# Performance work log

Hardware: AMD Instinct MI355X
Metric: run time of the kernel (lower is better)

## Reference

```python
import jax, jax.numpy as jnp
import numpy as np


def setup_inputs() -> dict:
    key = jax.random.key(0)
    kE, kD, kW, kU, kV = jax.random.split(key, 5)
    B, T, H, U = 32, 2048, 1024, 1024
    scale = 0.02
    return {
        "enc_out": jax.random.normal(kE, (B, T, H), dtype=jnp.float32),
        "dec_hidden": jax.random.normal(kD, (B, H), dtype=jnp.float32),
        "Wa": jax.random.normal(kW, (H, U), dtype=jnp.float32) * scale,
        "Ua": jax.random.normal(kU, (H, U), dtype=jnp.float32) * scale,
        "Va": jax.random.normal(kV, (U,), dtype=jnp.float32) * scale,
    }


def reference(enc_out, dec_hidden, Wa, Ua, Va):
    # Bahdanau additive attention.
    # enc_out: [B, T, H]; dec_hidden: [B, H]; Wa: [H, U]; Ua: [H, U]; Va: [U]
    dec_proj = jnp.einsum("bh,hu->bu", dec_hidden, Wa)          # [B, U]
    enc_proj = jnp.einsum("bth,hu->btu", enc_out, Ua)            # [B, T, U]
    s = jnp.tanh(enc_proj + dec_proj[:, None, :])                # [B, T, U]
    score = jnp.einsum("btu,u->bt", s, Va)                       # [B, T]
    alpha = jax.nn.softmax(score, axis=-1)                       # [B, T]
    context = jnp.einsum("bt,bth->bh", alpha, enc_out)           # [B, H]
    return context
```

## Files before the change

kernel.cpp:

```cpp
#include <hip/hip_runtime.h>
#include <stdint.h>


#define B_ 32
#define T_ 2048
#define H_ 1024
#define U_ 1024
#define M_ (B_ * T_)

typedef __bf16 bf16x8 __attribute__((ext_vector_type(8)));
typedef float f32x4 __attribute__((ext_vector_type(4)));

__device__ __forceinline__ unsigned f2b(float f) {
  unsigned u = __float_as_uint(f);
  return (u + 0x7FFFu + ((u >> 16) & 1u)) >> 16;
}
__device__ __forceinline__ float b2f(unsigned short u) {
  return __uint_as_float(((unsigned)u) << 16);
}
__device__ __forceinline__ float fast_tanh(float x) {
  float xc = fminf(fmaxf(x, -12.f), 12.f);
  float t = exp2f(xc * 2.885390081777927f);
  return (t - 1.f) * __builtin_amdgcn_rcpf(t + 1.f);
}

#define AS1 __attribute__((address_space(1)))
#define AS3 __attribute__((address_space(3)))
__device__ __forceinline__ void gld_lds16(const void* g, void* l) {
  __builtin_amdgcn_global_load_lds((AS1 const void*)g, (AS3 void*)l, 16, 0, 0);
}

__global__ __launch_bounds__(256) void conv_enc_k(const float4* __restrict__ in,
                                                  uint4* __restrict__ outA) {
  const int ml = threadIdx.x & 127, kh = threadIdx.x >> 7;
  const int bk = blockIdx.x;
  const int mt = blockIdx.y;
  const int kc = bk * 2 + kh;
  const float4* src = in + ((size_t)(mt * 128 + ml) * 256) + kc * 4;
  float4 a = src[0], b = src[1], c = src[2], d = src[3];
  uint4 o0, o1;
  o0.x = f2b(a.x) | (f2b(a.y) << 16);
  o0.y = f2b(a.z) | (f2b(a.w) << 16);
  o0.z = f2b(b.x) | (f2b(b.y) << 16);
  o0.w = f2b(b.z) | (f2b(b.w) << 16);
  o1.x = f2b(c.x) | (f2b(c.y) << 16);
  o1.y = f2b(c.z) | (f2b(c.w) << 16);
  o1.z = f2b(d.x) | (f2b(d.y) << 16);
  o1.w = f2b(d.z) | (f2b(d.w) << 16);
  const int k8 = kc * 2;
  outA[((size_t)mt * 128 + k8) * 128 + ml] = o0;
  outA[((size_t)mt * 128 + k8 + 1) * 128 + ml] = o1;
}

__global__ __launch_bounds__(256) void conv_ua_k(const float* __restrict__ in,
                                                 unsigned short* __restrict__ out) {
  int id = blockIdx.x * 256 + threadIdx.x;
  int h = id >> 10, u = id & 1023;
  out[(((size_t)(h >> 3) * U_ + u) << 3) + (h & 7)] = (unsigned short)f2b(in[id]);
}

__global__ __launch_bounds__(256) void decproj_k(const float* __restrict__ dh,
                                                 const float* __restrict__ Wa,
                                                 float* __restrict__ dp) {
  const int u = blockIdx.x * 256 + threadIdx.x;
  const int b = blockIdx.y, hz = blockIdx.z;
  const float* d = dh + b * H_ + hz * 256;
  const float* w = Wa + (size_t)(hz * 256) * U_ + u;
  float a0 = 0.f, a1 = 0.f, a2 = 0.f, a3 = 0.f;
#pragma unroll 4
  for (int h = 0; h < 256; h += 4) {
    a0 = fmaf(d[h + 0], w[(size_t)(h + 0) * U_], a0);
    a1 = fmaf(d[h + 1], w[(size_t)(h + 1) * U_], a1);
    a2 = fmaf(d[h + 2], w[(size_t)(h + 2) * U_], a2);
    a3 = fmaf(d[h + 3], w[(size_t)(h + 3) * U_], a3);
  }
  atomicAdd(&dp[b * U_ + u], (a0 + a1) + (a2 + a3));
}

__global__ __launch_bounds__(256, 2) void score_gemm_k(
    const unsigned short* __restrict__ encA,
    const unsigned short* __restrict__ Ub,
    const float* __restrict__ dp,
    const float* __restrict__ Va,
    float* __restrict__ score)
{
  __shared__ union {
    struct {
      alignas(16) unsigned short As[8][128][8];
      alignas(16) unsigned short Bs[8][128][8];
    } t;
    float sred[128 * 33];
  } sm;

  const int bx = blockIdx.x;
  const int mtile = bx & 511, ntile = bx >> 9;
  const int m0 = mtile << 7, n0 = ntile << 7;
  const int tid = threadIdx.x;
  const int wv = tid >> 6, ln = tid & 63;
  const int wm = wv & 1, wn = wv >> 1;
  const int quad = ln >> 4, l16 = ln & 15;

  f32x4 acc[4][4];
  const f32x4 zero = {0.f, 0.f, 0.f, 0.f};
#pragma unroll
  for (int i = 0; i < 4; ++i)
#pragma unroll
    for (int j = 0; j < 4; ++j) acc[i][j] = zero;

  const unsigned short* encT = encA + (size_t)mtile * (128 * 128 * 8);

  for (int k0 = 0; k0 < H_; k0 += 64) {
    __syncthreads();
#pragma unroll
    for (int c = 0; c < 4; ++c) {
      int chunk = (wv << 2) + c;
      int k8 = chunk >> 1, half = chunk & 1;
      const unsigned short* ga =
          encT + (((size_t)((k0 >> 3) + k8) * 128) + (half << 6) + ln) * 8;
      gld_lds16(ga, &sm.t.As[k8][half << 6][0]);
      const unsigned short* gb =
          Ub + (((size_t)((k0 >> 3) + k8) * U_) + n0 + (half << 6) + ln) * 8;
      gld_lds16(gb, &sm.t.Bs[k8][half << 6][0]);
    }
    __syncthreads();

#pragma unroll
    for (int kk = 0; kk < 2; ++kk) {
      int k8b = (kk << 2) + quad;
      bf16x8 af[4], bf[4];
#pragma unroll
      for (int mt = 0; mt < 4; ++mt)
        af[mt] = *(const bf16x8*)&sm.t.As[k8b][(wm << 6) + (mt << 4) + l16][0];
#pragma unroll
      for (int nt = 0; nt < 4; ++nt)
        bf[nt] = *(const bf16x8*)&sm.t.Bs[k8b][(wn << 6) + (nt << 4) + l16][0];
#pragma unroll
      for (int mt = 0; mt < 4; ++mt)
#pragma unroll
        for (int nt = 0; nt < 4; ++nt)
          acc[mt][nt] = __builtin_amdgcn_mfma_f32_16x16x32_bf16(
              af[mt], bf[nt], acc[mt][nt], 0, 0, 0);
    }
  }

  const int bq = m0 >> 11;
  float va[4], dpv[4];
#pragma unroll
  for (int nt = 0; nt < 4; ++nt) {
    int col = n0 + (wn << 6) + (nt << 4) + l16;
    va[nt] = Va[col];
    dpv[nt] = dp[bq * U_ + col];
  }
  __syncthreads();
#pragma unroll
  for (int mt = 0; mt < 4; ++mt) {
#pragma unroll
    for (int r = 0; r < 4; ++r) {
      float v = 0.f;
#pragma unroll
      for (int nt = 0; nt < 4; ++nt)
        v += fast_tanh(acc[mt][nt][r] + dpv[nt]) * va[nt];
      int row = (wm << 6) + (mt << 4) + (quad << 2) + r;
      sm.sred[row * 33 + (wn << 4) + l16] = v;
    }
  }
  __syncthreads();
  if (tid < 128) {
    const float* p = &sm.sred[tid * 33];
    float s = 0.f;
#pragma unroll
    for (int j = 0; j < 32; ++j) s += p[j];
    atomicAdd(&score[m0 + tid], s);
  }
}

__global__ __launch_bounds__(256) void softmax_k(float* __restrict__ score) {
  const int b = blockIdx.x, tid = threadIdx.x;
  float4* s4 = (float4*)(score + b * T_);
  __shared__ float red[4];
  float4 v0 = s4[tid * 2], v1 = s4[tid * 2 + 1];
  float m = fmaxf(fmaxf(fmaxf(v0.x, v0.y), fmaxf(v0.z, v0.w)),
                  fmaxf(fmaxf(v1.x, v1.y), fmaxf(v1.z, v1.w)));
#pragma unroll
  for (int off = 32; off >= 1; off >>= 1) m = fmaxf(m, __shfl_xor(m, off));
  if ((tid & 63) == 0) red[tid >> 6] = m;
  __syncthreads();
  m = fmaxf(fmaxf(red[0], red[1]), fmaxf(red[2], red[3]));
  __syncthreads();
  const float l2e = 1.4426950408889634f;
  float e[8];
  e[0] = exp2f((v0.x - m) * l2e); e[1] = exp2f((v0.y - m) * l2e);
  e[2] = exp2f((v0.z - m) * l2e); e[3] = exp2f((v0.w - m) * l2e);
  e[4] = exp2f((v1.x - m) * l2e); e[5] = exp2f((v1.y - m) * l2e);
  e[6] = exp2f((v1.z - m) * l2e); e[7] = exp2f((v1.w - m) * l2e);
  float sum = (e[0] + e[1]) + (e[2] + e[3]) + (e[4] + e[5]) + (e[6] + e[7]);
#pragma unroll
  for (int off = 32; off >= 1; off >>= 1) sum += __shfl_xor(sum, off);
  if ((tid & 63) == 0) red[tid >> 6] = sum;
  __syncthreads();
  float inv = 1.f / (red[0] + red[1] + red[2] + red[3]);
  v0.x = e[0] * inv; v0.y = e[1] * inv; v0.z = e[2] * inv; v0.w = e[3] * inv;
  v1.x = e[4] * inv; v1.y = e[5] * inv; v1.z = e[6] * inv; v1.w = e[7] * inv;
  s4[tid * 2] = v0;
  s4[tid * 2 + 1] = v1;
}

__global__ __launch_bounds__(256) void context_k(const uint4* __restrict__ encA,
                                                 const float* __restrict__ alpha,
                                                 float* __restrict__ out) {
  const int tx = threadIdx.x & 127, th = threadIdx.x >> 7;
  const int b = blockIdx.y, bt = blockIdx.x;
  const int mt = b * 16 + bt;
  const uint4* base = encA + ((size_t)mt * 128 + tx) * 128 + th * 64;
  const float* al = alpha + b * T_ + bt * 128 + th * 64;
  float a[8];
#pragma unroll
  for (int j = 0; j < 8; ++j) a[j] = 0.f;
#pragma unroll 4
  for (int i = 0; i < 64; ++i) {
    float w = al[i];
    uint4 e = base[i];
    a[0] = fmaf(w, b2f((unsigned short)e.x), a[0]);
    a[1] = fmaf(w, b2f((unsigned short)(e.x >> 16)), a[1]);
    a[2] = fmaf(w, b2f((unsigned short)e.y), a[2]);
    a[3] = fmaf(w, b2f((unsigned short)(e.y >> 16)), a[3]);
    a[4] = fmaf(w, b2f((unsigned short)e.z), a[4]);
    a[5] = fmaf(w, b2f((unsigned short)(e.z >> 16)), a[5]);
    a[6] = fmaf(w, b2f((unsigned short)e.w), a[6]);
    a[7] = fmaf(w, b2f((unsigned short)(e.w >> 16)), a[7]);
  }
  __shared__ float cred[2][128][8];
#pragma unroll
  for (int j = 0; j < 8; ++j) cred[th][tx][j] = a[j];
  __syncthreads();
  if (th == 0) {
#pragma unroll
    for (int j = 0; j < 8; ++j)
      atomicAdd(&out[b * H_ + tx * 8 + j], cred[0][tx][j] + cred[1][tx][j]);
  }
}

extern "C" void kernel_launch(void* const* d_in, const int* in_sizes, int n_in,
                              void* d_out, int out_size, void* d_ws, size_t ws_size,
                              hipStream_t stream) {
  const float* enc = (const float*)d_in[0];
  const float* dh  = (const float*)d_in[1];
  const float* Wa  = (const float*)d_in[2];
  const float* Ua  = (const float*)d_in[3];
  const float* Va  = (const float*)d_in[4];

  char* ws = (char*)d_ws;
  unsigned short* encA = (unsigned short*)ws;
  unsigned short* Ub   = (unsigned short*)(ws + 134217728);
  float* dp    = (float*)(ws + 134217728 + 2097152);
  float* score = (float*)(ws + 134217728 + 2097152 + 131072);

  hipMemsetAsync(dp, 0, B_ * U_ * sizeof(float), stream);
  hipMemsetAsync(score, 0, M_ * sizeof(float), stream);
  hipMemsetAsync(d_out, 0, B_ * H_ * sizeof(float), stream);

  conv_enc_k<<<dim3(32, 512), 256, 0, stream>>>((const float4*)enc, (uint4*)encA);
  conv_ua_k<<<4096, 256, 0, stream>>>(Ua, Ub);
  decproj_k<<<dim3(4, 32, 4), 256, 0, stream>>>(dh, Wa, dp);
  score_gemm_k<<<4096, 256, 0, stream>>>(encA, Ub, dp, Va, score);
  softmax_k<<<32, 256, 0, stream>>>(score);
  context_k<<<dim3(16, 32), 256, 0, stream>>>((const uint4*)encA, score, (float*)d_out);
}
```

Measured before the change: 626.9 us.

## Replace atomics with partial buffers and coalesce encoder bf16 conversion via LDS

Rewrites the encoder fp32-to-bf16 conversion so each block reads contiguous rows and writes the blocked layout through an LDS transpose, giving coalesced stores. All atomicAdd reductions (decoder projection, scores, context) are replaced by writes to per-split partial buffers that later kernels sum. This removes the three memsets and atomic contention, at the cost of an extra reduction kernel and more partial-buffer traffic. The workspace regions are reused: alpha aliases dp4 and ctxp aliases score8.

```diff
diff --git a/kernel.cpp b/kernel.cpp
--- a/kernel.cpp
+++ b/kernel.cpp
@@ -32,24 +32,32 @@
 
 __global__ __launch_bounds__(256) void conv_enc_k(const float4* __restrict__ in,
                                                   uint4* __restrict__ outA) {
-  const int ml = threadIdx.x & 127, kh = threadIdx.x >> 7;
-  const int bk = blockIdx.x;
-  const int mt = blockIdx.y;
-  const int kc = bk * 2 + kh;
-  const float4* src = in + ((size_t)(mt * 128 + ml) * 256) + kc * 4;
-  float4 a = src[0], b = src[1], c = src[2], d = src[3];
-  uint4 o0, o1;
-  o0.x = f2b(a.x) | (f2b(a.y) << 16);
-  o0.y = f2b(a.z) | (f2b(a.w) << 16);
-  o0.z = f2b(b.x) | (f2b(b.y) << 16);
-  o0.w = f2b(b.z) | (f2b(b.w) << 16);
-  o1.x = f2b(c.x) | (f2b(c.y) << 16);
-  o1.y = f2b(c.z) | (f2b(c.w) << 16);
-  o1.z = f2b(d.x) | (f2b(d.y) << 16);
-  o1.w = f2b(d.z) | (f2b(d.w) << 16);
-  const int k8 = kc * 2;
-  outA[((size_t)mt * 128 + k8) * 128 + ml] = o0;
-  outA[((size_t)mt * 128 + k8 + 1) * 128 + ml] = o1;
+  __shared__ uint4 L4[128 * 17];
+  const int tx = threadIdx.x;
+  const int band = blockIdx.x;
+  const int mt = band >> 3;
+  const int R = (band & 7) << 4;
+  const float4* src = in + (size_t)band * 4096;
+#pragma unroll
+  for (int i = 0; i < 8; ++i) {
+    int p = i * 256 + tx;
+    int r = p >> 7, pc = p & 127;
+    float4 a = src[r * 256 + pc * 2];
+    float4 b = src[r * 256 + pc * 2 + 1];
+    uint4 o;
+    o.x = f2b(a.x) | (f2b(a.y) << 16);
+    o.y = f2b(a.z) | (f2b(a.w) << 16);
+    o.z = f2b(b.x) | (f2b(b.y) << 16);
+    o.w = f2b(b.z) | (f2b(b.w) << 16);
+    L4[pc * 17 + r] = o;
+  }
+  __syncthreads();
+  const int r2 = tx & 15, kq = (tx >> 4) & 3, w = tx >> 6;
+#pragma unroll
+  for (int j = 0; j < 8; ++j) {
+    int k8 = j * 16 + w * 4 + kq;
+    outA[((size_t)mt * 128 + k8) * 128 + R + r2] = L4[k8 * 17 + r2];
+  }
 }
 
 __global__ __launch_bounds__(256) void conv_ua_k(const float* __restrict__ in,
@@ -61,7 +69,7 @@
 
 __global__ __launch_bounds__(256) void decproj_k(const float* __restrict__ dh,
                                                  const float* __restrict__ Wa,
-                                                 float* __restrict__ dp) {
+                                                 float* __restrict__ dp4) {
   const int u = blockIdx.x * 256 + threadIdx.x;
   const int b = blockIdx.y, hz = blockIdx.z;
   const float* d = dh + b * H_ + hz * 256;
@@ -74,15 +82,15 @@
     a2 = fmaf(d[h + 2], w[(size_t)(h + 2) * U_], a2);
     a3 = fmaf(d[h + 3], w[(size_t)(h + 3) * U_], a3);
   }
-  atomicAdd(&dp[b * U_ + u], (a0 + a1) + (a2 + a3));
+  dp4[((hz * B_ + b) * U_) + u] = (a0 + a1) + (a2 + a3);
 }
 
 __global__ __launch_bounds__(256, 2) void score_gemm_k(
     const unsigned short* __restrict__ encA,
     const unsigned short* __restrict__ Ub,
-    const float* __restrict__ dp,
+    const float* __restrict__ dp4,
     const float* __restrict__ Va,
-    float* __restrict__ score)
+    float* __restrict__ score8)
 {
   __shared__ union {
     struct {
@@ -149,7 +157,8 @@
   for (int nt = 0; nt < 4; ++nt) {
     int col = n0 + (wn << 6) + (nt << 4) + l16;
     va[nt] = Va[col];
-    dpv[nt] = dp[bq * U_ + col];
+    dpv[nt] = dp4[bq * U_ + col] + dp4[B_ * U_ + bq * U_ + col] +
+              dp4[2 * B_ * U_ + bq * U_ + col] + dp4[3 * B_ * U_ + bq * U_ + col];
   }
   __syncthreads();
 #pragma unroll
@@ -170,15 +179,22 @@
     float s = 0.f;
 #pragma unroll
     for (int j = 0; j < 32; ++j) s += p[j];
-    atomicAdd(&score[m0 + tid], s);
-  }
-}
-
-__global__ __launch_bounds__(256) void softmax_k(float* __restrict__ score) {
+    score8[(size_t)ntile * M_ + m0 + tid] = s;
+  }
+}
+
+__global__ __launch_bounds__(256) void softmax_k(const float* __restrict__ score8,
+                                                 float* __restrict__ alpha) {
   const int b = blockIdx.x, tid = threadIdx.x;
-  float4* s4 = (float4*)(score + b * T_);
   __shared__ float red[4];
-  float4 v0 = s4[tid * 2], v1 = s4[tid * 2 + 1];
+  float4 v0 = {0.f, 0.f, 0.f, 0.f}, v1 = {0.f, 0.f, 0.f, 0.f};
+#pragma unroll
+  for (int k = 0; k < 8; ++k) {
+    const float4* p = (const float4*)(score8 + (size_t)k * M_ + b * T_);
+    float4 x0 = p[tid * 2], x1 = p[tid * 2 + 1];
+    v0.x += x0.x; v0.y += x0.y; v0.z += x0.z; v0.w += x0.w;
+    v1.x += x1.x; v1.y += x1.y; v1.z += x1.z; v1.w += x1.w;
+  }
   float m = fmaxf(fmaxf(fmaxf(v0.x, v0.y), fmaxf(v0.z, v0.w)),
                   fmaxf(fmaxf(v1.x, v1.y), fmaxf(v1.z, v1.w)));
 #pragma unroll
@@ -199,15 +215,17 @@
   if ((tid & 63) == 0) red[tid >> 6] = sum;
   __syncthreads();
   float inv = 1.f / (red[0] + red[1] + red[2] + red[3]);
-  v0.x = e[0] * inv; v0.y = e[1] * inv; v0.z = e[2] * inv; v0.w = e[3] * inv;
-  v1.x = e[4] * inv; v1.y = e[5] * inv; v1.z = e[6] * inv; v1.w = e[7] * inv;
-  s4[tid * 2] = v0;
-  s4[tid * 2 + 1] = v1;
+  float4* a4 = (float4*)(alpha + b * T_);
+  float4 o0, o1;
+  o0.x = e[0] * inv; o0.y = e[1] * inv; o0.z = e[2] * inv; o0.w = e[3] * inv;
+  o1.x = e[4] * inv; o1.y = e[5] * inv; o1.z = e[6] * inv; o1.w = e[7] * inv;
+  a4[tid * 2] = o0;
+  a4[tid * 2 + 1] = o1;
 }
 
 __global__ __launch_bounds__(256) void context_k(const uint4* __restrict__ encA,
                                                  const float* __restrict__ alpha,
-                                                 float* __restrict__ out) {
+                                                 float* __restrict__ ctxp) {
   const int tx = threadIdx.x & 127, th = threadIdx.x >> 7;
   const int b = blockIdx.y, bt = blockIdx.x;
   const int mt = b * 16 + bt;
@@ -234,10 +252,20 @@
   for (int j = 0; j < 8; ++j) cred[th][tx][j] = a[j];
   __syncthreads();
   if (th == 0) {
-#pragma unroll
-    for (int j = 0; j < 8; ++j)
-      atomicAdd(&out[b * H_ + tx * 8 + j], cred[0][tx][j] + cred[1][tx][j]);
-  }
+    float* o = ctxp + (size_t)mt * H_ + tx * 8;
+#pragma unroll
+    for (int j = 0; j < 8; ++j) o[j] = cred[0][tx][j] + cred[1][tx][j];
+  }
+}
+
+__global__ __launch_bounds__(256) void ctx_red_k(const float* __restrict__ ctxp,
+                                                 float* __restrict__ out) {
+  int id = blockIdx.x * 256 + threadIdx.x;
+  int b = id >> 10, h = id & 1023;
+  float s = 0.f;
+#pragma unroll
+  for (int bt = 0; bt < 16; ++bt) s += ctxp[((size_t)(b * 16 + bt)) * H_ + h];
+  out[id] = s;
 }
 
 extern "C" void kernel_launch(void* const* d_in, const int* in_sizes, int n_in,
@@ -252,17 +280,16 @@
   char* ws = (char*)d_ws;
   unsigned short* encA = (unsigned short*)ws;
   unsigned short* Ub   = (unsigned short*)(ws + 134217728);
-  float* dp    = (float*)(ws + 134217728 + 2097152);
-  float* score = (float*)(ws + 134217728 + 2097152 + 131072);
-
-  hipMemsetAsync(dp, 0, B_ * U_ * sizeof(float), stream);
-  hipMemsetAsync(score, 0, M_ * sizeof(float), stream);
-  hipMemsetAsync(d_out, 0, B_ * H_ * sizeof(float), stream);
-
-  conv_enc_k<<<dim3(32, 512), 256, 0, stream>>>((const float4*)enc, (uint4*)encA);
+  float* dp4    = (float*)(ws + 136314880);
+  float* score8 = (float*)(ws + 136839168);
+  float* alpha  = dp4;
+  float* ctxp   = score8;
+
+  conv_enc_k<<<4096, 256, 0, stream>>>((const float4*)enc, (uint4*)encA);
   conv_ua_k<<<4096, 256, 0, stream>>>(Ua, Ub);
-  decproj_k<<<dim3(4, 32, 4), 256, 0, stream>>>(dh, Wa, dp);
-  score_gemm_k<<<4096, 256, 0, stream>>>(encA, Ub, dp, Va, score);
-  softmax_k<<<32, 256, 0, stream>>>(score);
-  context_k<<<dim3(16, 32), 256, 0, stream>>>((const uint4*)encA, score, (float*)d_out);
-}
+  decproj_k<<<dim3(4, 32, 4), 256, 0, stream>>>(dh, Wa, dp4);
+  score_gemm_k<<<4096, 256, 0, stream>>>(encA, Ub, dp4, Va, score8);
+  softmax_k<<<32, 256, 0, stream>>>(score8, alpha);
+  context_k<<<dim3(16, 32), 256, 0, stream>>>((const uint4*)encA, alpha, ctxp);
+  ctx_red_k<<<128, 256, 0, stream>>>(ctxp, (float*)d_out);
+}
```

After: 586.0 us. -6.5%, faster.
